# Performance work log

Hardware: AMD Instinct MI355X
Metric: run time of the kernel (lower is better)

Reference implementation:

```python
import jax, jax.numpy as jnp
import numpy as np

B, S, D, H, NC = 128, 256, 512, 1024, 128

def setup_inputs() -> dict:
    key = jax.random.key(0)
    ks = jax.random.split(key, 12)
    x = jax.random.randint(ks[0], (B, S, 1), 0, NC + 1)
    emb = jax.random.normal(ks[1], (NC + 1, D), dtype=jnp.float32)
    emb = emb.at[0].set(0.0)  # padding_idx=0
    def w(k, shape):
        return jax.random.normal(k, shape, dtype=jnp.float32) * (1.0 / np.sqrt(shape[0]))
    return {
        "x": x, "emb": emb,
        "Wfx": w(ks[2], (D, H)), "Wfh": w(ks[3], (H, H)), "bf": jnp.zeros(H),
        "Wix": w(ks[4], (D, H)), "Wih": w(ks[5], (H, H)), "bi": jnp.zeros(H),
        "Wgx": w(ks[6], (D, H)), "Wgh": w(ks[7], (H, H)), "bg": jnp.zeros(H),
        "Wox": w(ks[8], (D, H)), "Woh": w(ks[9], (H, H)), "bo": jnp.zeros(H),
        "Wph": w(ks[10], (H, NC)), "bp": jnp.zeros(NC),
    }

def reference(x, emb, Wfx, Wfh, bf, Wix, Wih, bi, Wgx, Wgh, bg, Wox, Woh, bo, Wph, bp):
    x_in = x[..., 0].astype(jnp.int32)            # [B,S]
    xe = emb[x_in]                                # [B,S,D]
    # Pre-compute the input-side gate projections for all timesteps (one big GEMM each).
    fx = jnp.einsum('bsd,dh->sbh', xe, Wfx) + bf
    ix = jnp.einsum('bsd,dh->sbh', xe, Wix) + bi
    gx = jnp.einsum('bsd,dh->sbh', xe, Wgx) + bg
    ox = jnp.einsum('bsd,dh->sbh', xe, Wox) + bo
    reset = (x_in > 0).astype(jnp.float32).T      # [S,B]
    def step(carry, inp):
        h, C = carry
        fx_t, ix_t, gx_t, ox_t, r_t = inp
        f = jax.nn.sigmoid(fx_t + h @ Wfh)
        i = jax.nn.sigmoid(ix_t + h @ Wih)
        g = jax.nn.sigmoid(gx_t + h @ Wgh)   # note: sigmoid (as in source), not tanh
        o = jax.nn.sigmoid(ox_t + h @ Woh)
        C = (g * i + C * f) * r_t[:, None]   # zero cell state on padding tokens
        h = o * jnp.tanh(C)
        return (h, C), None
    h0 = jnp.zeros((x.shape[0], Wfh.shape[0]), dtype=jnp.float32)
    (h, _), _ = jax.lax.scan(step, (h0, h0), (fx, ix, gx, ox, reset))
    p = h @ Wph + bp
    return jax.nn.log_softmax(p, axis=1)
```

## Files before the change

### kernel.cpp

```cpp
#include <hip/hip_runtime.h>
#include <hip/hip_bf16.h>

#define BB   128
#define SS   256
#define DD   512
#define HH   1024
#define NCC  128
#define NCLS 129
#define G4   4096
#define NWG  256

typedef __attribute__((ext_vector_type(8)))  short  short8;
typedef __attribute__((ext_vector_type(16))) float  f32x16;

static __device__ __forceinline__ float sigm(float x)  { return 1.0f / (1.0f + __expf(-x)); }
static __device__ __forceinline__ float tanh_(float x) { return 1.0f - 2.0f / (__expf(2.0f * x) + 1.0f); }
static __device__ __forceinline__ unsigned short f2b(float v) {
    __hip_bfloat16 h = __float2bfloat16(v);
    return *reinterpret_cast<unsigned short*>(&h);
}
static __device__ __forceinline__ short8 ld16(const unsigned short* p) {
    return *reinterpret_cast<const short8*>(p);
}

__global__ void k_pre(unsigned short* __restrict__ hb0, int* __restrict__ flags,
                      const float* __restrict__ Wfh, const float* __restrict__ Wih,
                      const float* __restrict__ Wgh, const float* __restrict__ Woh,
                      unsigned short* __restrict__ WhT,
                      const float* __restrict__ emb,
                      const float* __restrict__ Wfx, const float* __restrict__ Wix,
                      const float* __restrict__ Wgx, const float* __restrict__ Wox,
                      const float* __restrict__ bf_, const float* __restrict__ bi_,
                      const float* __restrict__ bg_, const float* __restrict__ bo_,
                      float* __restrict__ proj) {
    __shared__ float t[32][33];
    const int bid = blockIdx.x;
    if (bid < 512) {
        int i = bid * 256 + threadIdx.x;
        if (i < BB * HH) hb0[i] = 0;
        if (i < 16384) flags[i] = 0;
        return;
    }
    if (bid < 4608) {
        int b = bid - 512;
        int bx = b & 31, by = (b >> 5) & 31, g = b >> 10;
        const float* W = (g == 0) ? Wfh : (g == 1) ? Wih : (g == 2) ? Wgh : Woh;
        int h0 = bx * 32, k0 = by * 32;
        int tx = threadIdx.x & 31, ty = threadIdx.x >> 5;
        for (int r = 0; r < 4; r++) {
            int k = ty + r * 8;
            t[k][tx] = W[(size_t)(k0 + k) * HH + h0 + tx];
        }
        __syncthreads();
        for (int r = 0; r < 4; r++) {
            int hl = ty + r * 8;
            int j  = (h0 + hl) * 4 + g;
            WhT[(size_t)j * HH + k0 + tx] = f2b(t[tx][hl]);
        }
        return;
    }
    {
        int b = bid - 4608;
        int c = b >> 4;
        int j = (b & 15) * 256 + threadIdx.x;
        int hcol = j >> 2, g = j & 3;
        const float* Wx = (g == 0) ? Wfx : (g == 1) ? Wix : (g == 2) ? Wgx : Wox;
        const float* bb = (g == 0) ? bf_ : (g == 1) ? bi_ : (g == 2) ? bg_ : bo_;
        float acc = bb[hcol];
        const float* er = emb + (size_t)c * DD;
        for (int d = 0; d < DD; d++) acc += er[d] * Wx[(size_t)d * HH + hcol];
        proj[(size_t)c * G4 + j] = acc;
    }
}

#define LDAB(d, B, L) asm volatile("global_load_dwordx4 %0, %1, off offset:" L " sc0 sc1" \
                                   : "=v"(d) : "v"(B))
#define LD4(A, I) do { \
    LDAB(A[(I)+0], p, "0"); LDAB(A[(I)+1], p, "1024"); \
    LDAB(A[(I)+2], p, "2048"); LDAB(A[(I)+3], p, "3072"); p += 4096; } while (0)
#define LD16(A) do { LD4(A,0); LD4(A,4); LD4(A,8); LD4(A,12); } while (0)

#define WAITA(N, A) asm volatile("s_waitcnt vmcnt(" N ")" : \
    "+v"(A[0]),"+v"(A[1]),"+v"(A[2]),"+v"(A[3]),"+v"(A[4]),"+v"(A[5]),"+v"(A[6]),"+v"(A[7]), \
    "+v"(A[8]),"+v"(A[9]),"+v"(A[10]),"+v"(A[11]),"+v"(A[12]),"+v"(A[13]),"+v"(A[14]),"+v"(A[15]))

#define MF16(A, KB) do { \
    acc0 = __builtin_amdgcn_mfma_f32_32x32x16_bf16(A[0],  breg[(KB)+0],  acc0, 0,0,0); \
    acc1 = __builtin_amdgcn_mfma_f32_32x32x16_bf16(A[1],  breg[(KB)+1],  acc1, 0,0,0); \
    acc0 = __builtin_amdgcn_mfma_f32_32x32x16_bf16(A[2],  breg[(KB)+2],  acc0, 0,0,0); \
    acc1 = __builtin_amdgcn_mfma_f32_32x32x16_bf16(A[3],  breg[(KB)+3],  acc1, 0,0,0); \
    acc0 = __builtin_amdgcn_mfma_f32_32x32x16_bf16(A[4],  breg[(KB)+4],  acc0, 0,0,0); \
    acc1 = __builtin_amdgcn_mfma_f32_32x32x16_bf16(A[5],  breg[(KB)+5],  acc1, 0,0,0); \
    acc0 = __builtin_amdgcn_mfma_f32_32x32x16_bf16(A[6],  breg[(KB)+6],  acc0, 0,0,0); \
    acc1 = __builtin_amdgcn_mfma_f32_32x32x16_bf16(A[7],  breg[(KB)+7],  acc1, 0,0,0); \
    acc0 = __builtin_amdgcn_mfma_f32_32x32x16_bf16(A[8],  breg[(KB)+8],  acc0, 0,0,0); \
    acc1 = __builtin_amdgcn_mfma_f32_32x32x16_bf16(A[9],  breg[(KB)+9],  acc1, 0,0,0); \
    acc0 = __builtin_amdgcn_mfma_f32_32x32x16_bf16(A[10], breg[(KB)+10], acc0, 0,0,0); \
    acc1 = __builtin_amdgcn_mfma_f32_32x32x16_bf16(A[11], breg[(KB)+11], acc1, 0,0,0); \
    acc0 = __builtin_amdgcn_mfma_f32_32x32x16_bf16(A[12], breg[(KB)+12], acc0, 0,0,0); \
    acc1 = __builtin_amdgcn_mfma_f32_32x32x16_bf16(A[13], breg[(KB)+13], acc1, 0,0,0); \
    acc0 = __builtin_amdgcn_mfma_f32_32x32x16_bf16(A[14], breg[(KB)+14], acc0, 0,0,0); \
    acc1 = __builtin_amdgcn_mfma_f32_32x32x16_bf16(A[15], breg[(KB)+15], acc1, 0,0,0); \
} while (0)

#define PRLOAD(DSTA, CLSBUF) do { \
    _Pragma("unroll") \
    for (int r = 0; r < 16; r++) { \
        int row = (r & 3) + 8 * (r >> 2) + 4 * half; \
        const float* pa = proj + (size_t)CLSBUF[row] * G4 + jg; \
        asm volatile("global_load_dword %0, %1, off" : "=v"(DSTA[r]) \
                     : "v"((unsigned long long)pa)); \
    } \
} while (0)

__global__ __launch_bounds__(128, 1)
void k_scan(const int* __restrict__ x, const float* __restrict__ proj,
            const unsigned short* __restrict__ WhT,
            unsigned short* __restrict__ hb0, unsigned short* __restrict__ hb1,
            float* __restrict__ hf32, int* __restrict__ flags) {
    const int wg = blockIdx.x, tid = threadIdx.x;
    const int lane = tid & 63, wv = tid >> 6;
    const int l31 = lane & 31, half = lane >> 5;
    const int mg = wg & 3, ng = wg >> 2;
    const int m0 = mg * 32, n0 = ng * 64;
    const int jg = n0 + wv * 32 + l31;

    short8 breg[64];
    {
        const unsigned short* Bp = WhT + (size_t)jg * HH + half * 8;
        #pragma unroll
        for (int kk = 0; kk < 64; kk++) breg[kk] = ld16(Bp + kk * 16);
    }

    __shared__ float sg[32][68];
    __shared__ int   clsS[2][32];

    float Cst[4] = {0.0f, 0.0f, 0.0f, 0.0f};
    const int urow = tid & 31, uq = tid >> 5;

    if (tid < 32) clsS[0][tid] = x[(size_t)(m0 + tid) * SS];
    __syncthreads();

    const unsigned long long ab0 =
        (unsigned long long)((char*)hb0 + mg * 65536 + lane * 16);
    const unsigned long long ab1 =
        (unsigned long long)((char*)hb1 + mg * 65536 + lane * 16);
    const unsigned long long sb0 = (unsigned long long)((char*)hb0 + mg * 65536
        + ng * 1024 + (urow + ((uq >> 1) << 5)) * 16 + (uq & 1) * 8);
    const unsigned long long sb1 = (unsigned long long)((char*)hb1 + mg * 65536
        + ng * 1024 + (urow + ((uq >> 1) << 5)) * 16 + (uq & 1) * 8);

    const unsigned long long ctrAddr =
        (unsigned long long)(flags + (size_t)(8192 + mg * 32));

    float pr[16];
    PRLOAD(pr, clsS[0]);

    for (int s = 0; s < SS; s++) {
        const int cur = s & 1;
        unsigned long long p = cur ? ab1 : ab0;
        const unsigned long long sb = cur ? sb0 : sb1;

        short8 a0[16], a1[16], a2[16], a3[16];
        LD16(a0);
        LD16(a1);

        f32x16 acc0, acc1;
        #pragma unroll
        for (int r = 0; r < 16; r++) { acc0[r] = 0.0f; acc1[r] = 0.0f; }

        WAITA("16", a0);
        LD16(a2);
        MF16(a0, 0);
        WAITA("16", a1);
        LD16(a3);
        MF16(a1, 16);
        WAITA("16", a2);
        MF16(a2, 32);
        WAITA("0", a3);
        MF16(a3, 48);

        #pragma unroll
        for (int r = 0; r < 16; r++) {
            int row = (r & 3) + 8 * (r >> 2) + 4 * half;
            sg[row][wv * 32 + l31] = sigm(acc0[r] + acc1[r] + pr[r]);
        }
        __syncthreads();

        {
            const float rr = (clsS[cur][urow] > 0) ? 1.0f : 0.0f;
            unsigned short hv[4];
            #pragma unroll
            for (int q = 0; q < 4; q++) {
                float4 gq = *reinterpret_cast<const float4*>(&sg[urow][uq * 16 + q * 4]);
                float cn = (gq.z * gq.y + Cst[q] * gq.x) * rr;
                Cst[q] = cn;
                float hvv = gq.w * tanh_(cn);
                hv[q] = f2b(hvv);
                if (s == SS - 1)
                    hf32[(size_t)(m0 + urow) * HH + ng * 16 + uq * 4 + q] = hvv;
            }
            unsigned long long pk = (unsigned long long)hv[0]
                                  | ((unsigned long long)hv[1] << 16)
                                  | ((unsigned long long)hv[2] << 32)
                                  | ((unsigned long long)hv[3] << 48);
            asm volatile("global_store_dwordx2 %0, %1, off sc0 sc1" :: "v"(sb), "v"(pk) : "memory");
            if (s + 1 < SS && tid < 32)
                clsS[cur ^ 1][tid] = x[(size_t)(m0 + tid) * SS + s + 1];
        }

        if (s < SS - 1) {
            asm volatile("s_waitcnt vmcnt(0)" ::: "memory");
            __syncthreads();
            if (tid == 0) {
                int one = 1;
                asm volatile("global_atomic_add %0, %1, off"
                             :: "v"(ctrAddr), "v"(one) : "memory");
            }
            PRLOAD(pr, clsS[cur ^ 1]);
            const int tv = (s + 1) << 6;
            int got;
            do {
                asm volatile("global_load_dword %0, %1, off sc0 sc1\n\t"
                             "s_waitcnt vmcnt(0)"
                             : "=v"(got) : "v"(ctrAddr) : "memory");
            } while (got < tv);
        }
    }
}

__global__ void k_final(const float* __restrict__ hf32, const float* __restrict__ Wph,
                        const float* __restrict__ bp, float* __restrict__ out) {
    __shared__ float red[128];
    int b = blockIdx.x, c = threadIdx.x;
    const float* hr = hf32 + (size_t)b * HH;
    float acc = bp[c];
    for (int k = 0; k < HH; k++) acc += hr[k] * Wph[(size_t)k * NCC + c];
    red[c] = acc;
    __syncthreads();
    for (int st = 64; st > 0; st >>= 1) {
        if (c < st) red[c] = fmaxf(red[c], red[c + st]);
        __syncthreads();
    }
    float m = red[0];
    __syncthreads();
    red[c] = __expf(acc - m);
    __syncthreads();
    for (int st = 64; st > 0; st >>= 1) {
        if (c < st) red[c] += red[c + st];
        __syncthreads();
    }
    out[(size_t)b * NCC + c] = acc - m - __logf(red[0]);
}

extern "C" void kernel_launch(void* const* d_in, const int* in_sizes, int n_in,
                              void* d_out, int out_size, void* d_ws, size_t ws_size,
                              hipStream_t stream) {
    const int*   x   = (const int*)  d_in[0];
    const float* emb = (const float*)d_in[1];
    const float* Wfx = (const float*)d_in[2];
    const float* Wfh = (const float*)d_in[3];
    const float* bf_ = (const float*)d_in[4];
    const float* Wix = (const float*)d_in[5];
    const float* Wih = (const float*)d_in[6];
    const float* bi_ = (const float*)d_in[7];
    const float* Wgx = (const float*)d_in[8];
    const float* Wgh = (const float*)d_in[9];
    const float* bg_ = (const float*)d_in[10];
    const float* Wox = (const float*)d_in[11];
    const float* Woh = (const float*)d_in[12];
    const float* bo_ = (const float*)d_in[13];
    const float* Wph = (const float*)d_in[14];
    const float* bp_ = (const float*)d_in[15];
    float* out = (float*)d_out;

    char* ws = (char*)d_ws;
    unsigned short* WhT   = (unsigned short*)(ws);
    float*          proj  = (float*)(ws + 8388608);
    int*            flags = (int*)(ws + 10502656);
    unsigned short* hb0   = (unsigned short*)(ws + 10568192);
    unsigned short* hb1   = (unsigned short*)(ws + 10830336);
    float*          hf32  = (float*)(ws + 11092480);

    k_pre<<<dim3(6672), dim3(256), 0, stream>>>(hb0, flags, Wfh, Wih, Wgh, Woh, WhT,
                                                emb, Wfx, Wix, Wgx, Wox,
                                                bf_, bi_, bg_, bo_, proj);
    k_scan<<<dim3(NWG), dim3(128), 0, stream>>>(x, proj, WhT, hb0, hb1, hf32, flags);
    k_final<<<dim3(128), dim3(128), 0, stream>>>(hf32, Wph, bp_, out);
}
```

Baseline: 1.416 ms.

## Replace per-row atomic counter barrier with per-producer flags polled per K-chunk

```diff
diff --git a/kernel.cpp b/kernel.cpp
--- a/kernel.cpp
+++ b/kernel.cpp
@@ -113,6 +113,15 @@
     } \
 } while (0)
 
+#define POLLB(FA, OFF, TGT) do { \
+    int got; \
+    do { \
+        asm volatile("global_load_dword %0, %1, off offset:" OFF " sc0 sc1\n\t" \
+                     "s_waitcnt vmcnt(0)" \
+                     : "=v"(got) : "v"(FA) : "memory"); \
+    } while (__ballot(got >= (TGT)) != ~0ull); \
+} while (0)
+
 __global__ __launch_bounds__(128, 1)
 void k_scan(const int* __restrict__ x, const float* __restrict__ proj,
             const unsigned short* __restrict__ WhT,
@@ -150,8 +159,11 @@
     const unsigned long long sb1 = (unsigned long long)((char*)hb1 + mg * 65536
         + ng * 1024 + (urow + ((uq >> 1) << 5)) * 16 + (uq & 1) * 8);
 
-    const unsigned long long ctrAddr =
-        (unsigned long long)(flags + (size_t)(8192 + mg * 32));
+    const unsigned long long myFlag =
+        (unsigned long long)(flags + (size_t)(mg * 64 + ng) * 32);
+    const unsigned long long fpA =
+        (unsigned long long)(flags + (size_t)(mg * 64 + (lane & 15)) * 32);
+    const unsigned long long fpB = fpA + 4096;
 
     float pr[16];
     PRLOAD(pr, clsS[0]);
@@ -162,19 +174,22 @@
         const unsigned long long sb = cur ? sb0 : sb1;
 
         short8 a0[16], a1[16], a2[16], a3[16];
-        LD16(a0);
-        LD16(a1);
-
         f32x16 acc0, acc1;
         #pragma unroll
         for (int r = 0; r < 16; r++) { acc0[r] = 0.0f; acc1[r] = 0.0f; }
 
+        if (s > 0) POLLB(fpA, "0", s);
+        LD16(a0);
+        if (s > 0) POLLB(fpA, "2048", s);
+        LD16(a1);
         WAITA("16", a0);
+        MF16(a0, 0);
+        if (s > 0) POLLB(fpB, "0", s);
         LD16(a2);
-        MF16(a0, 0);
         WAITA("16", a1);
+        MF16(a1, 16);
+        if (s > 0) POLLB(fpB, "2048", s);
         LD16(a3);
-        MF16(a1, 16);
         WAITA("16", a2);
         MF16(a2, 32);
         WAITA("0", a3);
@@ -213,18 +228,11 @@
             asm volatile("s_waitcnt vmcnt(0)" ::: "memory");
             __syncthreads();
             if (tid == 0) {
-                int one = 1;
-                asm volatile("global_atomic_add %0, %1, off"
-                             :: "v"(ctrAddr), "v"(one) : "memory");
+                int fv = s + 1;
+                asm volatile("global_store_dword %0, %1, off sc0 sc1"
+                             :: "v"(myFlag), "v"(fv) : "memory");
             }
             PRLOAD(pr, clsS[cur ^ 1]);
-            const int tv = (s + 1) << 6;
-            int got;
-            do {
-                asm volatile("global_load_dword %0, %1, off sc0 sc1\n\t"
-                             "s_waitcnt vmcnt(0)"
-                             : "=v"(got) : "v"(ctrAddr) : "memory");
-            } while (got < tv);
         }
     }
 }
```

Result: slower. 1.551 ms (+9.6%).
